# Kernel tuning notes

Measured on AMD Instinct MI355X. Metric: run time of the kernel, lower is better.

## Reference

```python
import jax, jax.numpy as jnp
import numpy as np

EPS = 1e-5
NUM_HEADS = 8


def setup_inputs() -> dict:
    key = jax.random.key(0)
    ks = jax.random.split(key, 4)
    B, C, H, W = 16, 512, 32, 32
    x = jax.random.normal(ks[0], (B, C, H, W), dtype=jnp.float32)
    gn_w = jnp.ones((C,), dtype=jnp.float32)
    gn_b = jnp.zeros((C,), dtype=jnp.float32)
    # 1x1 conv weights stored as [out_ch, in_ch] (kernel dims squeezed)
    qkv_w = jax.random.normal(ks[1], (3 * C, C), dtype=jnp.float32) * (1.0 / np.sqrt(C))
    qkv_b = jnp.zeros((3 * C,), dtype=jnp.float32)
    proj_w = jax.random.normal(ks[2], (C, C), dtype=jnp.float32) * (1.0 / np.sqrt(C))
    proj_b = jnp.zeros((C,), dtype=jnp.float32)
    return {"x": x, "gn_w": gn_w, "gn_b": gn_b, "qkv_w": qkv_w,
            "qkv_b": qkv_b, "proj_w": proj_w, "proj_b": proj_b}


def _group_norm(x, w, b, groups):
    B, C, H, W = x.shape
    xg = x.reshape(B, groups, C // groups, H, W)
    mu = jnp.mean(xg, axis=(2, 3, 4), keepdims=True)
    var = jnp.var(xg, axis=(2, 3, 4), keepdims=True)
    xn = ((xg - mu) * jax.lax.rsqrt(var + EPS)).reshape(B, C, H, W)
    return xn * w[None, :, None, None] + b[None, :, None, None]


def reference(x, gn_w, gn_b, qkv_w, qkv_b, proj_w, proj_b):
    B, C, H, W = x.shape
    heads = NUM_HEADS
    d = C // heads
    residual = x
    xn = _group_norm(x, gn_w, gn_b, heads)
    # 1x1 conv == channel matmul
    qkv = jnp.einsum('oc,bchw->bohw', qkv_w, xn) + qkv_b[None, :, None, None]
    q, k, v = jnp.split(qkv, 3, axis=1)  # each [B, C, H, W]
    q = q.reshape(B, heads, d, H * W)
    k = k.reshape(B, heads, d, H * W)
    v = v.reshape(B, heads, d, H * W)
    scale = 1.0 / np.sqrt(d).astype(np.float32)
    attn = jnp.einsum('bhcn,bhcm->bhnm', q, k) * scale  # [B,h,N,N]
    attn = jax.nn.softmax(attn, axis=-1)
    out = jnp.einsum('bhnm,bhcm->bhcn', attn, v).reshape(B, C, H, W)
    out = jnp.einsum('oc,bchw->bohw', proj_w, out) + proj_b[None, :, None, None]
    return residual + out
```

## Files before the change

kernel.cpp:

```cpp
#include <hip/hip_runtime.h>
#include <hip/hip_bf16.h>
#include <math.h>

typedef short bf16x8 __attribute__((ext_vector_type(8)));
typedef float f32x4  __attribute__((ext_vector_type(4)));
#define MFMA16(a,b,c) __builtin_amdgcn_mfma_f32_16x16x32_bf16(a,b,c,0,0,0)

#define EPSF 1e-5f
#define QSC 0.18033688f

#if __has_builtin(__builtin_amdgcn_exp2f)
#define EXP2(x) __builtin_amdgcn_exp2f(x)
#else
#define EXP2(x) exp2f(x)
#endif

__device__ __forceinline__ unsigned int pk2n(float a, float b){
  __hip_bfloat162 h = __float22bfloat162_rn(make_float2(a, b));
  return *reinterpret_cast<unsigned int*>(&h);
}
__device__ __forceinline__ unsigned short bfn(float f){
  __hip_bfloat16 h = __float2bfloat16(f);
  return *reinterpret_cast<unsigned short*>(&h);
}
__device__ __forceinline__ float4 ld4(const float* p){ return *reinterpret_cast<const float4*>(p); }

__device__ __forceinline__ void gl_lds16(const unsigned short* g, unsigned short* l){
  __builtin_amdgcn_global_load_lds(
      (const __attribute__((address_space(1))) unsigned int*)g,
      (__attribute__((address_space(3))) unsigned int*)l, 16, 0, 0);
}

__global__ __launch_bounds__(512) void pre_k(const float* __restrict__ x,
                                             const float* __restrict__ gnw,
                                             const float* __restrict__ gnb,
                                             unsigned short* __restrict__ xnT,
                                             const float* __restrict__ qkvw,
                                             const float* __restrict__ projw,
                                             unsigned int* __restrict__ wqb,
                                             unsigned int* __restrict__ wpb){
  __shared__ float Xl[2][64*65];
  __shared__ float red[16];
  int blk = blockIdx.x;
  int tid = threadIdx.x;
  if(blk >= 128){
    const float* src; unsigned int* dst; int base;
    if(blk < 320){ src = qkvw; dst = wqb; base = 128; }
    else         { src = projw; dst = wpb; base = 320; }
    int i = (blk - base)*1024 + tid*2;
    #pragma unroll
    for(int j = 0; j < 2; j++){
      float4 v = reinterpret_cast<const float4*>(src)[i + j];
      uint2 r; r.x = pk2n(v.x, v.y); r.y = pk2n(v.z, v.w);
      reinterpret_cast<uint2*>(dst)[i + j] = r;
    }
    return;
  }
  int b = blk >> 3, g = blk & 7;
  const float4* p4 = reinterpret_cast<const float4*>(x + (size_t)blk * 65536);
  float s1 = 0.f, s2 = 0.f;
  for(int i = tid; i < 16384; i += 512){
    float4 v = p4[i];
    s1 += (v.x + v.y) + (v.z + v.w);
    s2 += v.x*v.x + v.y*v.y + v.z*v.z + v.w*v.w;
  }
  #pragma unroll
  for(int off = 32; off; off >>= 1){ s1 += __shfl_xor(s1, off); s2 += __shfl_xor(s2, off); }
  if((tid & 63) == 0){ red[tid >> 6] = s1; red[8 + (tid >> 6)] = s2; }
  __syncthreads();
  float a = 0.f, b2 = 0.f;
  #pragma unroll
  for(int w = 0; w < 8; w++){ a += red[w]; b2 += red[8 + w]; }
  float mean = a * (1.f / 65536.f);
  float rstd = rsqrtf(b2 * (1.f / 65536.f) - mean * mean + EPSF);
  int half = tid >> 8, t256 = tid & 255;
  int nq = t256 & 15, rr = t256 >> 4;
  int c0 = g * 64;
  for(int it = 0; it < 8; it++){
    int n0 = (it*2 + half) * 64;
    __syncthreads();
    #pragma unroll
    for(int p = 0; p < 4; p++){
      int cl = p * 16 + rr, c = c0 + cl;
      float s = rstd * gnw[c], t = gnb[c] - mean * s;
      float4 v = ld4(x + ((size_t)(b*512 + c))*1024 + n0 + 4*nq);
      Xl[half][(4*nq+0)*65 + cl] = v.x*s + t;
      Xl[half][(4*nq+1)*65 + cl] = v.y*s + t;
      Xl[half][(4*nq+2)*65 + cl] = v.z*s + t;
      Xl[half][(4*nq+3)*65 + cl] = v.w*s + t;
    }
    __syncthreads();
    int n = t256 >> 2, cq = t256 & 3;
    float f[16];
    #pragma unroll
    for(int k = 0; k < 16; k++) f[k] = Xl[half][n*65 + 16*cq + k];
    uint4 w0, w1;
    w0.x = pk2n(f[0],f[1]);  w0.y = pk2n(f[2],f[3]);  w0.z = pk2n(f[4],f[5]);  w0.w = pk2n(f[6],f[7]);
    w1.x = pk2n(f[8],f[9]);  w1.y = pk2n(f[10],f[11]);w1.z = pk2n(f[12],f[13]);w1.w = pk2n(f[14],f[15]);
    unsigned short* dp = xnT + ((size_t)(b*1024 + n0 + n))*512 + c0 + 16*cq;
    *reinterpret_cast<uint4*>(dp)     = w0;
    *reinterpret_cast<uint4*>(dp + 8) = w1;
  }
}


__global__ __launch_bounds__(256) void qkv_mm(const unsigned short* __restrict__ A,
                                              const unsigned short* __restrict__ Bx,
                                              const float* __restrict__ bias,
                                              unsigned short* __restrict__ T,
                                              unsigned short* __restrict__ V){
  __shared__ __align__(16) unsigned short As[2][128*64], Bs[2][128*64];
  int tid = threadIdx.x;
  int n0 = blockIdx.x*128, o0 = blockIdx.y*128, b = blockIdx.z;
  int wid = tid >> 6, wr = wid >> 1, wc = wid & 1, ln = tid & 15, g = (tid >> 4) & 3;
  int l = tid & 63;
  int rsw = (ln & 7) << 3;
  int srow = 32*wid + (l >> 3);
  int scol = (((l & 7) ^ (l >> 3)) << 3);
  const unsigned short* Ag = A  + (size_t)(o0 + srow)*512 + scol;
  const unsigned short* Bg = Bx + ((size_t)(b*1024 + n0 + srow))*512 + scol;
  f32x4 acc[4][4] = {};
  #pragma unroll
  for(int c = 0; c < 4; c++){
    gl_lds16(Ag + (size_t)(8*c)*512, &As[0][(32*wid + 8*c)*64]);
    gl_lds16(Bg + (size_t)(8*c)*512, &Bs[0][(32*wid + 8*c)*64]);
  }
  for(int t = 0; t < 8; t++){
    int buf = t & 1;
    if(t < 7){
      int k1 = (t + 1) * 64;
      #pragma unroll
      for(int c = 0; c < 4; c++){
        gl_lds16(Ag + (size_t)(8*c)*512 + k1, &As[buf^1][(32*wid + 8*c)*64]);
        gl_lds16(Bg + (size_t)(8*c)*512 + k1, &Bs[buf^1][(32*wid + 8*c)*64]);
      }
      asm volatile("s_waitcnt vmcnt(8)" ::: "memory");
    } else {
      asm volatile("s_waitcnt vmcnt(0)" ::: "memory");
    }
    __builtin_amdgcn_sched_barrier(0);
    __builtin_amdgcn_s_barrier();
    __builtin_amdgcn_sched_barrier(0);
    #pragma unroll
    for(int kh = 0; kh < 2; kh++){
      int ro = (kh*32 + 8*g) ^ rsw;
      bf16x8 af[4], bfv[4];
      #pragma unroll
      for(int mf = 0; mf < 4; mf++)
        af[mf] = *reinterpret_cast<const bf16x8*>(&As[buf][(wr*64 + 16*mf + ln)*64 + ro]);
      #pragma unroll
      for(int nf = 0; nf < 4; nf++)
        bfv[nf] = *reinterpret_cast<const bf16x8*>(&Bs[buf][(wc*64 + 16*nf + ln)*64 + ro]);
      #pragma unroll
      for(int mf = 0; mf < 4; mf++)
        #pragma unroll
        for(int nf = 0; nf < 4; nf++)
          acc[mf][nf] = MFMA16(af[mf], bfv[nf], acc[mf][nf]);
    }
    __builtin_amdgcn_sched_barrier(0);
    __builtin_amdgcn_s_barrier();
  }
  int obase = o0 + wr*64, nbase = n0 + wc*64;
  unsigned short* scr = &As[0][0] + wid * 2560;
  float sc = (obase < 512) ? QSC : 1.0f;
  if(obase < 1024){
    #pragma unroll
    for(int h2 = 0; h2 < 2; h2++){
      asm volatile("s_waitcnt lgkmcnt(0)" ::: "memory");
      __builtin_amdgcn_sched_barrier(0);
      #pragma unroll
      for(int mf2 = 0; mf2 < 2; mf2++){
        int mf = 2*h2 + mf2;
        int og = obase + 16*mf + 4*g;
        float b0 = bias[og], b1 = bias[og+1], b2 = bias[og+2], b3 = bias[og+3];
        #pragma unroll
        for(int nf = 0; nf < 4; nf++){
          uint2 pr;
          pr.x = pk2n((acc[mf][nf][0]+b0)*sc, (acc[mf][nf][1]+b1)*sc);
          pr.y = pk2n((acc[mf][nf][2]+b2)*sc, (acc[mf][nf][3]+b3)*sc);
          *reinterpret_cast<uint2*>(&scr[(16*nf + ln)*40 + 16*mf2 + 4*g]) = pr;
        }
      }
      asm volatile("s_waitcnt lgkmcnt(0)" ::: "memory");
      __builtin_amdgcn_sched_barrier(0);
      const unsigned short* rp = &scr[l*40];
      uint4 r0 = *reinterpret_cast<const uint4*>(rp);
      uint4 r1 = *reinterpret_cast<const uint4*>(rp+8);
      uint4 r2 = *reinterpret_cast<const uint4*>(rp+16);
      uint4 r3 = *reinterpret_cast<const uint4*>(rp+24);
      unsigned short* dp = T + ((size_t)(b*1024 + nbase + l))*1024 + obase + 32*h2;
      *reinterpret_cast<uint4*>(dp)    = r0;
      *reinterpret_cast<uint4*>(dp+8)  = r1;
      *reinterpret_cast<uint4*>(dp+16) = r2;
      *reinterpret_cast<uint4*>(dp+24) = r3;
    }
  } else {
    #pragma unroll
    for(int h2 = 0; h2 < 2; h2++){
      asm volatile("s_waitcnt lgkmcnt(0)" ::: "memory");
      __builtin_amdgcn_sched_barrier(0);
      #pragma unroll
      for(int nf2 = 0; nf2 < 2; nf2++){
        int nf = 2*h2 + nf2;
        #pragma unroll
        for(int mf = 0; mf < 4; mf++){
          int og = obase + 16*mf + 4*g;
          #pragma unroll
          for(int r = 0; r < 4; r++)
            scr[(16*mf + 4*g + r)*40 + 16*nf2 + ln] = bfn(acc[mf][nf][r] + bias[og+r]);
        }
      }
      asm volatile("s_waitcnt lgkmcnt(0)" ::: "memory");
      __builtin_amdgcn_sched_barrier(0);
      const unsigned short* rp = &scr[l*40];
      uint4 r0 = *reinterpret_cast<const uint4*>(rp);
      uint4 r1 = *reinterpret_cast<const uint4*>(rp+8);
      uint4 r2 = *reinterpret_cast<const uint4*>(rp+16);
      uint4 r3 = *reinterpret_cast<const uint4*>(rp+24);
      unsigned short* dp = V + ((size_t)(b*512 + obase - 1024 + l))*1024 + nbase + 32*h2;
      *reinterpret_cast<uint4*>(dp)    = r0;
      *reinterpret_cast<uint4*>(dp+8)  = r1;
      *reinterpret_cast<uint4*>(dp+16) = r2;
      *reinterpret_cast<uint4*>(dp+24) = r3;
    }
  }
}

__global__ __launch_bounds__(256) void attn_bf_k(const unsigned short* __restrict__ T,
                                                 const unsigned short* __restrict__ V,
                                                 unsigned short* __restrict__ attT){
  __shared__ __align__(16) unsigned short KT[2][64*64];
  __shared__ __align__(16) unsigned short Vt[2][64*64];
  __shared__ __align__(16) unsigned int   Pl[4*16*32];
  int tid = threadIdx.x;
  int id = blockIdx.x;
  int bh = (id >> 7) * 8 + (id & 7);
  int n0 = ((id >> 3) & 15) * 64;
  int b = bh >> 3, h = bh & 7;
  int wq = tid >> 6, ln = tid & 15, g = (tid >> 4) & 3;
  int l = tid & 63;
  int nl = n0 + wq*16 + ln;
  const unsigned short* Tb = T + ((size_t)b << 20);
  bf16x8 qf0 = *reinterpret_cast<const bf16x8*>(Tb + (size_t)nl*1024 + h*64 + 8*g);
  bf16x8 qf1 = *reinterpret_cast<const bf16x8*>(Tb + (size_t)nl*1024 + h*64 + 32 + 8*g);
  f32x4 acc[4] = {};
  float l_part = 0.f;
  const unsigned short* kg = Tb + 512 + h*64;
  const unsigned short* vg = V + ((size_t)(b*512 + h*64))*1024;
  int pbase = wq*512 + ln*32;
  int psw = (ln & 7) << 2;
  int swz  = (((l & 7) << 3) ^ ((l >> 3) << 3));
  const unsigned short* ksrc = kg + (size_t)(wq*16 + (l>>3))*1024 + swz;
  const unsigned short* vsrc = vg + (size_t)(wq*16 + (l>>3))*1024 + swz;
  int rsw = (ln & 7) << 3;
  int ro0 = (8*g) ^ rsw, ro1 = (32 + 8*g) ^ rsw;
  {
    unsigned short* kb = &KT[0][wq*16*64];
    unsigned short* vb = &Vt[0][wq*16*64];
    gl_lds16(ksrc,            kb);
    gl_lds16(ksrc + 8*1024,   kb + 8*64);
    gl_lds16(vsrc,            vb);
    gl_lds16(vsrc + 8*1024,   vb + 8*64);
  }
  __syncthreads();
  for(int t = 0; t < 16; t++){
    int buf = t & 1;
    if(t < 15){
      int m1 = (t + 1) * 64;
      unsigned short* kb = &KT[buf^1][wq*16*64];
      unsigned short* vb = &Vt[buf^1][wq*16*64];
      gl_lds16(ksrc + (size_t)m1*1024,          kb);
      gl_lds16(ksrc + (size_t)(m1+8)*1024,      kb + 8*64);
      gl_lds16(vsrc + m1,                       vb);
      gl_lds16(vsrc + 8*1024 + m1,              vb + 8*64);
    }
    f32x4 sf[4];
    #pragma unroll
    for(int mf = 0; mf < 4; mf++){
      bf16x8 a0 = *reinterpret_cast<const bf16x8*>(&KT[buf][(16*mf + ln)*64 + ro0]);
      bf16x8 a1 = *reinterpret_cast<const bf16x8*>(&KT[buf][(16*mf + ln)*64 + ro1]);
      f32x4 z = {0.f, 0.f, 0.f, 0.f};
      z = MFMA16(a0, qf0, z);
      sf[mf] = MFMA16(a1, qf1, z);
    }
    float p[16];
    #pragma unroll
    for(int mf = 0; mf < 4; mf++)
      #pragma unroll
      for(int r = 0; r < 4; r++){
        float v = EXP2(sf[mf][r]);
        p[mf*4 + r] = v;
        l_part += v;
      }
    #pragma unroll
    for(int mt = 0; mt < 4; mt++){
      Pl[pbase + ((8*mt + 2*g + 0) ^ psw)] = pk2n(p[4*mt + 0], p[4*mt + 1]);
      Pl[pbase + ((8*mt + 2*g + 1) ^ psw)] = pk2n(p[4*mt + 2], p[4*mt + 3]);
    }
    asm volatile("s_waitcnt lgkmcnt(0)" ::: "memory");
    __builtin_amdgcn_sched_barrier(0);
    union { uint4 u; bf16x8 hv; } pb0, pb1;
    pb0.u = *reinterpret_cast<const uint4*>(&Pl[pbase + ((4*g) ^ psw)]);
    pb1.u = *reinterpret_cast<const uint4*>(&Pl[pbase + ((16 + 4*g) ^ psw)]);
    #pragma unroll
    for(int cf = 0; cf < 4; cf++){
      bf16x8 v0 = *reinterpret_cast<const bf16x8*>(&Vt[buf][(16*cf + ln)*64 + ro0]);
      bf16x8 v1 = *reinterpret_cast<const bf16x8*>(&Vt[buf][(16*cf + ln)*64 + ro1]);
      acc[cf] = MFMA16(v0, pb0.hv, acc[cf]);
      acc[cf] = MFMA16(v1, pb1.hv, acc[cf]);
    }
    __syncthreads();
  }
  float lsum = l_part;
  lsum += __shfl_xor(lsum, 16);
  lsum += __shfl_xor(lsum, 32);
  float inv = 1.f / lsum;
  unsigned short* op = attT + ((size_t)(b*1024 + nl))*512 + h*64;
  #pragma unroll
  for(int cf = 0; cf < 4; cf++){
    uint2 pr;
    pr.x = pk2n(acc[cf][0]*inv, acc[cf][1]*inv);
    pr.y = pk2n(acc[cf][2]*inv, acc[cf][3]*inv);
    *reinterpret_cast<uint2*>(op + 16*cf + 4*g) = pr;
  }
}

__global__ __launch_bounds__(256) void proj_mm(const unsigned short* __restrict__ A,
                                               const unsigned short* __restrict__ Bx,
                                               const float* __restrict__ bias,
                                               const float* __restrict__ resid,
                                               float* __restrict__ out){
  __shared__ __align__(16) unsigned short As[2][128*64], Bs[2][128*64];
  int tid = threadIdx.x;
  int n0 = blockIdx.x*128, o0 = blockIdx.y*128, b = blockIdx.z;
  int wid = tid >> 6, wr = wid >> 1, wc = wid & 1, ln = tid & 15, g = (tid >> 4) & 3;
  int l = tid & 63;
  int rsw = (ln & 7) << 3;
  int srow = 32*wid + (l >> 3);
  int scol = (((l & 7) ^ (l >> 3)) << 3);
  const unsigned short* Ag = A  + (size_t)(o0 + srow)*512 + scol;
  const unsigned short* Bg = Bx + ((size_t)(b*1024 + n0 + srow))*512 + scol;
  f32x4 acc[4][4] = {};
  #pragma unroll
  for(int c = 0; c < 4; c++){
    gl_lds16(Ag + (size_t)(8*c)*512, &As[0][(32*wid + 8*c)*64]);
    gl_lds16(Bg + (size_t)(8*c)*512, &Bs[0][(32*wid + 8*c)*64]);
  }
  for(int t = 0; t < 8; t++){
    int buf = t & 1;
    if(t < 7){
      int k1 = (t + 1) * 64;
      #pragma unroll
      for(int c = 0; c < 4; c++){
        gl_lds16(Ag + (size_t)(8*c)*512 + k1, &As[buf^1][(32*wid + 8*c)*64]);
        gl_lds16(Bg + (size_t)(8*c)*512 + k1, &Bs[buf^1][(32*wid + 8*c)*64]);
      }
      asm volatile("s_waitcnt vmcnt(8)" ::: "memory");
    } else {
      asm volatile("s_waitcnt vmcnt(0)" ::: "memory");
    }
    __builtin_amdgcn_sched_barrier(0);
    __builtin_amdgcn_s_barrier();
    __builtin_amdgcn_sched_barrier(0);
    #pragma unroll
    for(int kh = 0; kh < 2; kh++){
      int ro = (kh*32 + 8*g) ^ rsw;
      bf16x8 af[4], bfv[4];
      #pragma unroll
      for(int mf = 0; mf < 4; mf++)
        af[mf] = *reinterpret_cast<const bf16x8*>(&As[buf][(wr*64 + 16*mf + ln)*64 + ro]);
      #pragma unroll
      for(int nf = 0; nf < 4; nf++)
        bfv[nf] = *reinterpret_cast<const bf16x8*>(&Bs[buf][(wc*64 + 16*nf + ln)*64 + ro]);
      #pragma unroll
      for(int mf = 0; mf < 4; mf++)
        #pragma unroll
        for(int nf = 0; nf < 4; nf++)
          acc[mf][nf] = MFMA16(af[mf], bfv[nf], acc[mf][nf]);
    }
    __builtin_amdgcn_sched_barrier(0);
    __builtin_amdgcn_s_barrier();
  }
  #pragma unroll
  for(int mf = 0; mf < 4; mf++)
    #pragma unroll
    for(int r = 0; r < 4; r++){
      int o = o0 + wr*64 + 16*mf + 4*g + r;
      float bo = bias[o];
      #pragma unroll
      for(int nf = 0; nf < 4; nf++){
        int n = n0 + wc*64 + 16*nf + ln;
        size_t off = ((size_t)(b*512 + o))*1024 + n;
        out[off] = acc[mf][nf][r] + bo + resid[off];
      }
    }
}

extern "C" void kernel_launch(void* const* d_in, const int* in_sizes, int n_in,
                              void* d_out, int out_size, void* d_ws, size_t ws_size,
                              hipStream_t stream){
  const float* x     = (const float*)d_in[0];
  const float* gnw   = (const float*)d_in[1];
  const float* gnb   = (const float*)d_in[2];
  const float* qkvw  = (const float*)d_in[3];
  const float* qkvb  = (const float*)d_in[4];
  const float* projw = (const float*)d_in[5];
  const float* projb = (const float*)d_in[6];
  float* out = (float*)d_out;

  char* w = (char*)d_ws;
  unsigned short* wqb = (unsigned short*)w;  w += (size_t)1536*512*2;
  unsigned short* wpb = (unsigned short*)w;  w += (size_t)512*512*2;
  unsigned short* xnT = (unsigned short*)w;  w += (size_t)16*1024*512*2;
  unsigned short* Tqk = (unsigned short*)w;  w += (size_t)16*1024*1024*2;
  unsigned short* Vb  = (unsigned short*)w;  w += (size_t)16*512*1024*2;
  unsigned short* attT = (unsigned short*)w; w += (size_t)16*1024*512*2;

  hipLaunchKernelGGL(pre_k, dim3(384), dim3(512), 0, stream,
                     x, gnw, gnb, xnT, qkvw, projw,
                     (unsigned int*)wqb, (unsigned int*)wpb);
  hipLaunchKernelGGL(qkv_mm, dim3(8, 12, 16), dim3(256), 0, stream, wqb, xnT, qkvb, Tqk, Vb);
  hipLaunchKernelGGL(attn_bf_k, dim3(2048), dim3(256), 0, stream, Tqk, Vb, attT);
  hipLaunchKernelGGL(proj_mm, dim3(8, 4, 16), dim3(256), 0, stream, wpb, attT, projb, x, out);
}
```

Before: 147.8 us.

## Load K fragments directly into registers and relax per-iteration barrier wait

The attention kernel stops staging K tiles through shared memory. Each wave now loads its K MFMA fragments straight from global memory into registers, prefetching the next tile after the QK MFMAs. The end-of-iteration __syncthreads is replaced by a partial vmcnt wait plus a raw s_barrier, so the K register prefetch can stay in flight across the barrier. This removes LDS traffic and LDS space for K, but every wave now loads all 64 K rows itself (four times the global/L2 traffic for K). It also relies on a hand-tuned vmcnt count being correct.

```diff
diff --git a/kernel.cpp b/kernel.cpp
--- a/kernel.cpp
+++ b/kernel.cpp
@@ -229,7 +229,6 @@
 __global__ __launch_bounds__(256) void attn_bf_k(const unsigned short* __restrict__ T,
                                                  const unsigned short* __restrict__ V,
                                                  unsigned short* __restrict__ attT){
-  __shared__ __align__(16) unsigned short KT[2][64*64];
   __shared__ __align__(16) unsigned short Vt[2][64*64];
   __shared__ __align__(16) unsigned int   Pl[4*16*32];
   int tid = threadIdx.x;
@@ -250,38 +249,45 @@
   int pbase = wq*512 + ln*32;
   int psw = (ln & 7) << 2;
   int swz  = (((l & 7) << 3) ^ ((l >> 3) << 3));
-  const unsigned short* ksrc = kg + (size_t)(wq*16 + (l>>3))*1024 + swz;
   const unsigned short* vsrc = vg + (size_t)(wq*16 + (l>>3))*1024 + swz;
   int rsw = (ln & 7) << 3;
   int ro0 = (8*g) ^ rsw, ro1 = (32 + 8*g) ^ rsw;
   {
-    unsigned short* kb = &KT[0][wq*16*64];
     unsigned short* vb = &Vt[0][wq*16*64];
-    gl_lds16(ksrc,            kb);
-    gl_lds16(ksrc + 8*1024,   kb + 8*64);
     gl_lds16(vsrc,            vb);
     gl_lds16(vsrc + 8*1024,   vb + 8*64);
+  }
+  bf16x8 ka0[4], ka1[4];
+  #pragma unroll
+  for(int mf = 0; mf < 4; mf++){
+    const unsigned short* kr = kg + (size_t)(16*mf + ln)*1024 + 8*g;
+    ka0[mf] = *reinterpret_cast<const bf16x8*>(kr);
+    ka1[mf] = *reinterpret_cast<const bf16x8*>(kr + 32);
   }
   __syncthreads();
   for(int t = 0; t < 16; t++){
     int buf = t & 1;
     if(t < 15){
       int m1 = (t + 1) * 64;
-      unsigned short* kb = &KT[buf^1][wq*16*64];
       unsigned short* vb = &Vt[buf^1][wq*16*64];
-      gl_lds16(ksrc + (size_t)m1*1024,          kb);
-      gl_lds16(ksrc + (size_t)(m1+8)*1024,      kb + 8*64);
-      gl_lds16(vsrc + m1,                       vb);
-      gl_lds16(vsrc + 8*1024 + m1,              vb + 8*64);
+      gl_lds16(vsrc + m1,            vb);
+      gl_lds16(vsrc + 8*1024 + m1,   vb + 8*64);
     }
     f32x4 sf[4];
     #pragma unroll
     for(int mf = 0; mf < 4; mf++){
-      bf16x8 a0 = *reinterpret_cast<const bf16x8*>(&KT[buf][(16*mf + ln)*64 + ro0]);
-      bf16x8 a1 = *reinterpret_cast<const bf16x8*>(&KT[buf][(16*mf + ln)*64 + ro1]);
       f32x4 z = {0.f, 0.f, 0.f, 0.f};
-      z = MFMA16(a0, qf0, z);
-      sf[mf] = MFMA16(a1, qf1, z);
+      z = MFMA16(ka0[mf], qf0, z);
+      sf[mf] = MFMA16(ka1[mf], qf1, z);
+    }
+    if(t < 15){
+      int m1 = (t + 1) * 64;
+      #pragma unroll
+      for(int mf = 0; mf < 4; mf++){
+        const unsigned short* kr = kg + (size_t)(m1 + 16*mf + ln)*1024 + 8*g;
+        ka0[mf] = *reinterpret_cast<const bf16x8*>(kr);
+        ka1[mf] = *reinterpret_cast<const bf16x8*>(kr + 32);
+      }
     }
     float p[16];
     #pragma unroll
@@ -309,7 +315,12 @@
       acc[cf] = MFMA16(v0, pb0.hv, acc[cf]);
       acc[cf] = MFMA16(v1, pb1.hv, acc[cf]);
     }
-    __syncthreads();
+    if(t < 15){
+      __builtin_amdgcn_sched_barrier(0);
+      asm volatile("s_waitcnt vmcnt(8)" ::: "memory");
+      __builtin_amdgcn_sched_barrier(0);
+      __builtin_amdgcn_s_barrier();
+    }
   }
   float lsum = l_part;
   lsum += __shfl_xor(lsum, 16);
```

Result: slower. 215.0 us (+45.5%).
